# Performance work log

Measured on AMD Instinct MI355X. Metric: run time of the kernel, lower is better.

The kernel has to match this reference:

```python
import jax, jax.numpy as jnp
import numpy as np

B, S, NH, HID, NL = 64, 512, 16, 512, 16
W_WIN, PAD, THR, BW = 5, 2, 5.0, 0.1
D_IN = 1 + 2 * NH


def setup_inputs():
    key = jax.random.key(0)
    ks = jax.random.split(key, 16)
    time = jax.random.uniform(ks[0], (B, S)) * 1000.0
    mag = 15.0 + jax.random.normal(ks[1], (B, S))
    err = 0.01 + 0.1 * jax.random.uniform(ks[2], (B, S))
    sc = 0.05
    p = {}
    p["light_curve"] = jnp.stack([time, mag, err], axis=1)  # (B,3,S)
    p["valid_mask"] = jnp.ones((B, S), dtype=bool)
    p["frequency"] = 0.5 + 4.5 * jax.random.uniform(ks[3], (B,))
    p["W_ih0"] = sc * jax.random.normal(ks[4], (3 * HID, D_IN))
    p["b_ih0"] = jnp.zeros((3 * HID,))
    p["W_hh0"] = sc * jax.random.normal(ks[5], (3 * HID, HID))
    p["b_hh0"] = jnp.zeros((3 * HID,))
    p["W_ih1"] = sc * jax.random.normal(ks[6], (3 * HID, HID))
    p["b_ih1"] = jnp.zeros((3 * HID,))
    p["W_hh1"] = sc * jax.random.normal(ks[7], (3 * HID, HID))
    p["b_hh1"] = jnp.zeros((3 * HID,))
    p["Wl1"] = sc * jax.random.normal(ks[8], (HID, HID))
    p["bl1"] = jnp.zeros((HID,))
    p["Wl2"] = sc * jax.random.normal(ks[9], (NL, HID))
    p["bl2"] = jnp.zeros((NL,))
    return p


def _flag_outliers(phase, mag):
    # Sorted-window weighted (Epanechnikov in circular phase-delta) mean/std outlier test.
    # Caller guarantees all points valid (setup uses an all-True mask), so index_select == identity.
    perm = jnp.argsort(phase)
    ps, ms = phase[perm], mag[perm]

    def windows(x):
        xp = jnp.concatenate([x[-PAD:], x, x[:PAD]])  # circular pad
        return jnp.stack([xp[i:i + S] for i in range(W_WIN)], axis=-1)  # (S, w)

    wp, wm = windows(ps), windows(ms)
    cols = jnp.array([i for i in range(W_WIN) if i != PAD])
    dphi = wp[:, cols] - wp[:, PAD:PAD + 1]
    dphi = jnp.remainder(dphi - 0.5, 1.0) - 0.5
    wgt = 0.75 * (1.0 - dphi ** 2)
    wmm = wm[:, cols]
    wsum = wgt.sum(-1)
    loc = (wmm * wgt).sum(-1) / wsum
    scale = jnp.sqrt((((wmm - loc[:, None]) ** 2) * wgt).sum(-1) / (wsum - 1.0))
    thr = loc + THR * scale
    sigma = jnp.zeros_like(mag).at[perm].set(thr)  # inverse-permute (index_copy_)
    return mag > sigma


def _gru_layer(x, W_ih, b_ih, W_hh, b_hh):
    # torch nn.GRU cell math; x: (B,S,D) -> (B,S,H)
    xW = jnp.einsum('bsd,gd->bsg', x, W_ih) + b_ih  # (B,S,3H)

    def step(h, xt):
        hW = h @ W_hh.T + b_hh
        xr, xz, xn = jnp.split(xt, 3, axis=-1)
        hr, hz, hn = jnp.split(hW, 3, axis=-1)
        r = jax.nn.sigmoid(xr + hr)
        z = jax.nn.sigmoid(xz + hz)
        n = jnp.tanh(xn + r * hn)
        h = (1.0 - z) * n + z * h
        return h, h

    h0 = jnp.zeros((x.shape[0], W_hh.shape[1]), x.dtype)
    _, hs = jax.lax.scan(step, h0, jnp.swapaxes(xW, 0, 1))
    return jnp.swapaxes(hs, 0, 1)


def reference(light_curve, valid_mask, frequency, W_ih0, b_ih0, W_hh0, b_hh0,
              W_ih1, b_ih1, W_hh1, b_hh1, Wl1, bl1, Wl2, bl2):
    time, mag, err = light_curve[:, 0], light_curve[:, 1], light_curve[:, 2]
    period = 2.0 / frequency[:, None]  # fold_with_double_period=True (default)
    phase = jnp.remainder(time, period) / period
    outlier = jax.vmap(_flag_outliers)(phase, mag)
    is_valid = valid_mask & ~outlier

    # periodic-kernel interpolation on 50-point grid; align phase to brightness max
    grid = jnp.linspace(0.0, 1.0, 50)
    delta = grid[None, :, None] - phase[:, None, :]  # (B,50,S)
    K = jnp.exp((jnp.cos(2.0 * jnp.pi * delta) - 1.0) / BW ** 2)
    Wk = is_valid[:, None, :].astype(K.dtype) * K
    Wk = Wk / Wk.sum(-1, keepdims=True)
    smooth = (Wk * mag[:, None, :]).sum(-1)  # (B,50)
    phase = phase - grid[jnp.argmax(smooth, axis=-1)][:, None]

    # sort by phase, invalid points last; scaler=None -> loc 0, scale 1
    big = jnp.finfo(jnp.float32).max
    idx = jnp.argsort(jnp.where(is_valid, phase, big), axis=-1)
    phase = jnp.take_along_axis(phase, idx, -1)
    mag = jnp.take_along_axis(mag, idx, -1)
    is_valid = jnp.take_along_axis(is_valid, idx, -1)

    # Fourier phase embedding [cos_1..cos_H, sin_1..sin_H] + mag -> (B,S,2H+1)
    k = jnp.arange(1, NH + 1, dtype=phase.dtype)
    ang = 2.0 * jnp.pi * phase[:, :, None] * k
    emb = jnp.concatenate([jnp.cos(ang), jnp.sin(ang), mag[:, :, None]], axis=-1)

    ht = _gru_layer(emb, W_ih0, b_ih0, W_hh0, b_hh0)
    ht = _gru_layer(ht, W_ih1, b_ih1, W_hh1, b_hh1)

    m = is_valid[:, :, None].astype(ht.dtype)  # context='average'
    ctx = (ht * m).sum(1) / m.sum(1)
    h1 = jax.nn.gelu(ctx @ Wl1.T + bl1, approximate=False)
    z = h1 @ Wl2.T + bl2
    return z
```

## Files before the change

### kernel.cpp

```cpp
#include <hip/hip_runtime.h>


typedef unsigned short u16;
typedef unsigned int u32;
typedef unsigned long long u64;

__device__ __forceinline__ float b2f(u16 u) { return __uint_as_float(((u32)u) << 16); }
__device__ __forceinline__ float blo(u32 u) { return __uint_as_float(u << 16); }
__device__ __forceinline__ float bhi(u32 u) { return __uint_as_float(u & 0xffff0000u); }
__device__ __forceinline__ u16 f2b(float f) {
    u32 x = __float_as_uint(f);
    u32 r = x + 0x7fffu + ((x >> 16) & 1u);
    return (u16)(r >> 16);
}

#define SS 512
#define TWO_PI 6.28318530717958647692f
#define BIGF 3.402823466e+38f
#define PANEL_ELEMS (1536 * 512)
#define FLAGS_BYTES 32768
#define RD 4

struct P {
    const void* lc;
    const void* freq;
    const void* W[12];
    void* out;
    void* ws;
    unsigned long long ws_size;
};

__device__ __forceinline__ bool inputs_are_bf16(const void* freq) {
    const u16* q = (const u16*)freq;
    bool ok = true;
    for (int i = 0; i < 64; ++i) {
        float v = b2f(q[i]);
        ok = ok && (v >= 0.4f) && (v <= 5.5f);
    }
    return ok;
}

template<bool BF>
__device__ __forceinline__ float ldw(const void* p, size_t i) {
    if constexpr (BF) return b2f(((const u16*)p)[i]);
    else              return ((const float*)p)[i];
}
template<bool BF>
__device__ __forceinline__ const void* rowp(const void* base, int row) {
    if constexpr (BF) return (const void*)((const u16*)base + (size_t)row * 512);
    else              return (const void*)((const float*)base + (size_t)row * 512);
}

__device__ __forceinline__ void sc_store_f(float* ptr, float v) {
    __hip_atomic_store(ptr, v, __ATOMIC_RELAXED, __HIP_MEMORY_SCOPE_AGENT);
}
__device__ __forceinline__ float sc_load_f(const float* ptr) {
    return __hip_atomic_load(ptr, __ATOMIC_RELAXED, __HIP_MEMORY_SCOPE_AGENT);
}
__device__ __forceinline__ void sc_store_i(int* ptr, int v) {
    __hip_atomic_store(ptr, v, __ATOMIC_RELAXED, __HIP_MEMORY_SCOPE_AGENT);
}
__device__ __forceinline__ int sc_load_i(const int* ptr) {
    return __hip_atomic_load(ptr, __ATOMIC_RELAXED, __HIP_MEMORY_SCOPE_AGENT);
}

__device__ __forceinline__ void waitge(const int* f, int v, int* dead) {
    if (*dead) return;
    int it = 0;
    while (sc_load_i(f) < v) {
        __builtin_amdgcn_s_sleep(1);
        if (++it > 2000000) { *dead = 1; break; }
    }
}

template<bool BF>
__device__ void build_panel_one(const void* W, int tid, char* panbase) {
    if constexpr (BF) {
        const uint4* Ws = (const uint4*)W;
        uint4* panel = (uint4*)panbase;
        for (int i = tid; i < 1536 * 64; i += 512) {
            int r = i >> 6, k8 = i & 63;
            panel[(size_t)k8 * 1536 + r] = Ws[i];
        }
    } else {
        const float4* Ws = (const float4*)W;
        float4* panel = (float4*)panbase;
        for (int i = tid; i < 1536 * 128; i += 512) {
            int r = i >> 7, k4 = i & 127;
            panel[(size_t)k4 * 1536 + r] = Ws[i];
        }
    }
}

template<bool BF>
__device__ __forceinline__ void tridot_panel(const void* panel, int j,
                                             const float* __restrict__ sh,
                                             float& ar, float& az, float& an) {
    if constexpr (BF) {
        const uint4* pr = (const uint4*)panel + j;
        const uint4* pz = pr + 512;
        const uint4* pn = pr + 1024;
        for (int k0 = 0; k0 < 512; k0 += 8) {
            size_t o = (size_t)(k0 >> 3) * 1536;
            float4 h0 = *(const float4*)&sh[k0];
            float4 h1 = *(const float4*)&sh[k0 + 4];
            uint4 a = pr[o], c = pz[o], d = pn[o];
            ar += blo(a.x) * h0.x + bhi(a.x) * h0.y + blo(a.y) * h0.z + bhi(a.y) * h0.w
                + blo(a.z) * h1.x + bhi(a.z) * h1.y + blo(a.w) * h1.z + bhi(a.w) * h1.w;
            az += blo(c.x) * h0.x + bhi(c.x) * h0.y + blo(c.y) * h0.z + bhi(c.y) * h0.w
                + blo(c.z) * h1.x + bhi(c.z) * h1.y + blo(c.w) * h1.z + bhi(c.w) * h1.w;
            an += blo(d.x) * h0.x + bhi(d.x) * h0.y + blo(d.y) * h0.z + bhi(d.y) * h0.w
                + blo(d.z) * h1.x + bhi(d.z) * h1.y + blo(d.w) * h1.z + bhi(d.w) * h1.w;
        }
    } else {
        const float4* pr = (const float4*)panel + j;
        const float4* pz = pr + 512;
        const float4* pn = pr + 1024;
        for (int k0 = 0; k0 < 512; k0 += 8) {
            size_t o = (size_t)(k0 >> 2) * 1536;
            float4 h0 = *(const float4*)&sh[k0];
            float4 h1 = *(const float4*)&sh[k0 + 4];
            float4 a0 = pr[o], a1 = pr[o + 1536];
            float4 c0 = pz[o], c1 = pz[o + 1536];
            float4 d0 = pn[o], d1 = pn[o + 1536];
            ar += a0.x * h0.x + a0.y * h0.y + a0.z * h0.z + a0.w * h0.w
                + a1.x * h1.x + a1.y * h1.y + a1.z * h1.z + a1.w * h1.w;
            az += c0.x * h0.x + c0.y * h0.y + c0.z * h0.z + c0.w * h0.w
                + c1.x * h1.x + c1.y * h1.y + c1.z * h1.z + c1.w * h1.w;
            an += d0.x * h0.x + d0.y * h0.y + d0.z * h0.z + d0.w * h0.w
                + d1.x * h1.x + d1.y * h1.y + d1.z * h1.z + d1.w * h1.w;
        }
    }
}

template<bool BF>
__device__ __forceinline__ float dot512(const void* vr, const float* __restrict__ sh) {
    float acc = 0.f;
    if constexpr (BF) {
        const u32* pr = (const u32*)vr;
        for (int k0 = 0; k0 < 512; k0 += 8) {
            float4 h0 = *(const float4*)&sh[k0];
            float4 h1 = *(const float4*)&sh[k0 + 4];
            uint4 a = *(const uint4*)(pr + (k0 >> 1));
            acc += blo(a.x) * h0.x + bhi(a.x) * h0.y + blo(a.y) * h0.z + bhi(a.y) * h0.w
                 + blo(a.z) * h1.x + bhi(a.z) * h1.y + blo(a.w) * h1.z + bhi(a.w) * h1.w;
        }
    } else {
        const float* pr = (const float*)vr;
        for (int k0 = 0; k0 < 512; k0 += 8) {
            float4 h0 = *(const float4*)&sh[k0];
            float4 h1 = *(const float4*)&sh[k0 + 4];
            float4 a0 = *(const float4*)(pr + k0), a1 = *(const float4*)(pr + k0 + 4);
            acc += a0.x * h0.x + a0.y * h0.y + a0.z * h0.z + a0.w * h0.w
                 + a1.x * h1.x + a1.y * h1.y + a1.z * h1.z + a1.w * h1.w;
        }
    }
    return acc;
}

struct PreShm {
    float ph[512], mg[512], skey[512], sig[512], vld[512];
    int   sidx[512];
    float ps2[512], ms2[512], vs2[512];
    float pn[50][8], pd[50][8], smoothv[50];
    float gshift, nv;
};

__device__ void bitonic512(float* skey, int* sidx, int tid) {
    for (int k = 2; k <= 512; k <<= 1) {
        for (int j = k >> 1; j > 0; j >>= 1) {
            int ixj = tid ^ j;
            if (ixj > tid) {
                float ka = skey[tid], kb = skey[ixj];
                int ia = sidx[tid], ib = sidx[ixj];
                bool up = ((tid & k) == 0);
                bool agtb = (ka > kb) || (ka == kb && ia > ib);
                if (agtb == up) {
                    skey[tid] = kb; skey[ixj] = ka;
                    sidx[tid] = ib; sidx[ixj] = ia;
                }
            }
            __syncthreads();
        }
    }
}

template<bool BF>
__device__ void preproc_core(const P& p, PreShm& s, int b, int tid) {
    float period = 2.0f / ldw<BF>(p.freq, b);
    float t = ldw<BF>(p.lc, (size_t)b * 3 * SS + tid);
    float m = ldw<BF>(p.lc, (size_t)b * 3 * SS + SS + tid);
    float ph0 = fmodf(t, period) / period;
    s.ph[tid] = ph0; s.mg[tid] = m;
    s.skey[tid] = ph0; s.sidx[tid] = tid;
    __syncthreads();
    bitonic512(s.skey, s.sidx, tid);
    {
        float pc = s.skey[tid];
        float wv[4], mv[4];
        float wsum = 0.f, wm = 0.f;
        const int offs[4] = {-2, -1, 1, 2};
#pragma unroll
        for (int c = 0; c < 4; ++c) {
            int jj = (tid + offs[c]) & 511;
            float d = s.skey[jj] - pc;
            float u = d - 0.5f; u = u - floorf(u);
            float dphi = u - 0.5f;
            float w = 0.75f * (1.0f - dphi * dphi);
            float mm = s.mg[s.sidx[jj]];
            wv[c] = w; mv[c] = mm;
            wsum += w; wm += w * mm;
        }
        float loc = wm / wsum;
        float s2 = 0.f;
#pragma unroll
        for (int c = 0; c < 4; ++c) { float dm = mv[c] - loc; s2 += dm * dm * wv[c]; }
        float scale = sqrtf(s2 / (wsum - 1.0f));
        s.sig[s.sidx[tid]] = loc + 5.0f * scale;
    }
    __syncthreads();
    s.vld[tid] = (s.mg[tid] > s.sig[tid]) ? 0.0f : 1.0f;
    __syncthreads();
    if (tid == 0) {
        float acc = 0.f;
        for (int i = 0; i < 512; ++i) acc += s.vld[i];
        s.nv = acc;
    }
    {
        int g = tid >> 3, pq = tid & 7;
        if (g < 50) {
            float gv = (float)g * (1.0f / 49.0f);
            float num = 0.f, den = 0.f;
            int s0 = pq * 64;
            for (int ss = s0; ss < s0 + 64; ++ss) {
                float d = gv - s.ph[ss];
                float c = cosf(TWO_PI * d);
                float K = expf((c - 1.0f) * 100.0f);
                float w = s.vld[ss] * K;
                den += w; num += w * s.mg[ss];
            }
            s.pn[g][pq] = num; s.pd[g][pq] = den;
        }
    }
    __syncthreads();
    if (tid < 50) {
        float num = 0.f, den = 0.f;
#pragma unroll
        for (int c = 0; c < 8; ++c) { num += s.pn[tid][c]; den += s.pd[tid][c]; }
        s.smoothv[tid] = num / den;
    }
    __syncthreads();
    if (tid == 0) {
        float best = s.smoothv[0]; int bi = 0;
        for (int g = 1; g < 50; ++g) if (s.smoothv[g] > best) { best = s.smoothv[g]; bi = g; }
        s.gshift = (float)bi * (1.0f / 49.0f);
    }
    __syncthreads();
    float p2 = s.ph[tid] - s.gshift;
    s.ph[tid] = p2;
    s.skey[tid] = (s.vld[tid] > 0.f) ? p2 : BIGF;
    s.sidx[tid] = tid;
    __syncthreads();
    bitonic512(s.skey, s.sidx, tid);
    {
        int o = s.sidx[tid];
        s.ps2[tid] = s.ph[o]; s.ms2[tid] = s.mg[o]; s.vs2[tid] = s.vld[o];
    }
    __syncthreads();
}

struct ShmU {
    union {
        struct { PreShm pre; float h0[512], h1[512], eL[34]; } a;
        struct { float h0loc[512]; } b;
        struct { float vs2[512], h1[512], cg[1024], nv; } c;
    } u;
    int dead;
};

template<bool BF, bool PAN>
__device__ void run_all(const P& p, ShmU& S) {
    PreShm& pre = S.u.a.pre;
    float* h0 = S.u.a.h0;
    float* h1 = S.u.a.h1;
    float* eL = S.u.a.eL;
    int b = blockIdx.x, tid = threadIdx.x;
    char* panbase = (char*)p.ws + FLAGS_BYTES;
    const size_t PMAT = (size_t)PANEL_ELEMS * (BF ? 2 : 4);

    if constexpr (PAN) {
        build_panel_one<BF>(p.W[2], tid, panbase);
        build_panel_one<BF>(p.W[4], tid, panbase + PMAT);
        build_panel_one<BF>(p.W[6], tid, panbase + 2 * PMAT);
        __threadfence();
    }
    preproc_core<BF>(p, pre, b, tid);

    int j = tid;
    float wr0[33], wz0[33], wn0[33];
#pragma unroll
    for (int d = 0; d < 33; ++d) {
        wr0[d] = ldw<BF>(p.W[0], (size_t)j * 33 + d);
        wz0[d] = ldw<BF>(p.W[0], ((size_t)j + 512) * 33 + d);
        wn0[d] = ldw<BF>(p.W[0], ((size_t)j + 1024) * 33 + d);
    }
    float bi0r = ldw<BF>(p.W[1], j), bi0z = ldw<BF>(p.W[1], j + 512), bi0n = ldw<BF>(p.W[1], j + 1024);
    float bh0r = ldw<BF>(p.W[3], j), bh0z = ldw<BF>(p.W[3], j + 512), bh0n = ldw<BF>(p.W[3], j + 1024);
    float bi1r = ldw<BF>(p.W[5], j), bi1z = ldw<BF>(p.W[5], j + 512), bi1n = ldw<BF>(p.W[5], j + 1024);
    float bh1r = ldw<BF>(p.W[7], j), bh1z = ldw<BF>(p.W[7], j + 512), bh1n = ldw<BF>(p.W[7], j + 1024);

    const void* pan0  = (const void*)panbase;
    const void* pan1x = (const void*)(panbase + PMAT);
    const void* pan1h = (const void*)(panbase + 2 * PMAT);
    const void *w0r = rowp<BF>(p.W[2], j), *w0z = rowp<BF>(p.W[2], j + 512), *w0n = rowp<BF>(p.W[2], j + 1024);
    const void *x1r = rowp<BF>(p.W[4], j), *x1z = rowp<BF>(p.W[4], j + 512), *x1n = rowp<BF>(p.W[4], j + 1024);
    const void *w1r = rowp<BF>(p.W[6], j), *w1z = rowp<BF>(p.W[6], j + 512), *w1n = rowp<BF>(p.W[6], j + 1024);

    h0[j] = 0.f; h1[j] = 0.f;
    float cacc = 0.f;
    __syncthreads();

    for (int tt = 0; tt < 512; ++tt) {
        if (j < 16) {
            float ang = TWO_PI * pre.ps2[tt] * (float)(j + 1);
            float sv, cv; sincosf(ang, &sv, &cv);
            eL[j] = cv; eL[16 + j] = sv;
        }
        if (j == 32) eL[32] = pre.ms2[tt];
        __syncthreads();
        float xr = bi0r, xz = bi0z, xn = bi0n;
#pragma unroll
        for (int d = 0; d < 33; ++d) {
            float e = eL[d];
            xr += wr0[d] * e; xz += wz0[d] * e; xn += wn0[d] * e;
        }
        float ar = bh0r, az = bh0z, an = bh0n;
        if constexpr (PAN) tridot_panel<BF>(pan0, j, h0, ar, az, an);
        else {
            for (int k = 0; k < 512; ++k) {
                float h = h0[k];
                ar += ldw<BF>(w0r, k) * h; az += ldw<BF>(w0z, k) * h; an += ldw<BF>(w0n, k) * h;
            }
        }
        float h0prev = h0[j];
        float r0 = 1.0f / (1.0f + expf(-(xr + ar)));
        float z0 = 1.0f / (1.0f + expf(-(xz + az)));
        float n0 = tanhf(xn + r0 * an);
        float nh0 = (1.0f - z0) * n0 + z0 * h0prev;
        __syncthreads();
        h0[j] = nh0;
        __syncthreads();
        float yr = bi1r, yz = bi1z, yn = bi1n;
        float cr = bh1r, cz = bh1z, cn = bh1n;
        if constexpr (PAN) {
            tridot_panel<BF>(pan1x, j, h0, yr, yz, yn);
            tridot_panel<BF>(pan1h, j, h1, cr, cz, cn);
        } else {
            for (int k = 0; k < 512; ++k) {
                float h = h0[k], g = h1[k];
                yr += ldw<BF>(x1r, k) * h; yz += ldw<BF>(x1z, k) * h; yn += ldw<BF>(x1n, k) * h;
                cr += ldw<BF>(w1r, k) * g; cz += ldw<BF>(w1z, k) * g; cn += ldw<BF>(w1n, k) * g;
            }
        }
        float h1prev = h1[j];
        float r1 = 1.0f / (1.0f + expf(-(yr + cr)));
        float z1 = 1.0f / (1.0f + expf(-(yz + cz)));
        float n1 = tanhf(yn + r1 * cn);
        float nh1 = (1.0f - z1) * n1 + z1 * h1prev;
        cacc += pre.vs2[tt] * nh1;
        __syncthreads();
        h1[j] = nh1;
    }
    __syncthreads();

    h0[j] = cacc / pre.nv;
    __syncthreads();
    float a1 = ldw<BF>(p.W[9], j) + dot512<BF>(rowp<BF>(p.W[8], j), h0);
    float g = 0.5f * a1 * (1.0f + erff(a1 * 0.70710678118654752440f));
    __syncthreads();
    h1[j] = g;
    __syncthreads();
    if (j < 16) {
        float a2 = ldw<BF>(p.W[11], j) + dot512<BF>(rowp<BF>(p.W[10], j), h1);
        if constexpr (BF) ((u16*)p.out)[(size_t)b * 16 + j] = f2b(a2);
        else              ((float*)p.out)[(size_t)b * 16 + j] = a2;
    }
}

__global__ __launch_bounds__(512) void fused_kernel_old(P p) {
    __shared__ ShmU S;
    bool bf = inputs_are_bf16(p.freq);
    u64 PMAT = bf ? 1572864ull : 3145728ull;
    bool pan = (p.ws && p.ws_size >= (u64)FLAGS_BYTES + 3 * PMAT);
    if (bf) { if (pan) run_all<true, true>(p, S);  else run_all<true, false>(p, S); }
    else    { if (pan) run_all<false, true>(p, S); else run_all<false, false>(p, S); }
}


template<bool BF>
__device__ void runA(const P& p, ShmU& S, int b, int tid,
                     char* panbase, float* h0r, float* vs2g, float* nvg, int* flags) {
    build_panel_one<BF>(p.W[2], tid, panbase);
    __threadfence();
    preproc_core<BF>(p, S.u.a.pre, b, tid);
    sc_store_f(&vs2g[(size_t)b * 512 + tid], S.u.a.pre.vs2[tid]);
    if (tid == 0) sc_store_f(&nvg[b], S.u.a.pre.nv);
    asm volatile("s_waitcnt vmcnt(0)" ::: "memory");
    __syncthreads();
    if (tid == 0) { S.dead = 0; sc_store_i(&flags[4096 + b * 16], 1); }

    int j = tid;
    float wr0[33], wz0[33], wn0[33];
#pragma unroll
    for (int d = 0; d < 33; ++d) {
        wr0[d] = ldw<BF>(p.W[0], (size_t)j * 33 + d);
        wz0[d] = ldw<BF>(p.W[0], ((size_t)j + 512) * 33 + d);
        wn0[d] = ldw<BF>(p.W[0], ((size_t)j + 1024) * 33 + d);
    }
    float bi0r = ldw<BF>(p.W[1], j), bi0z = ldw<BF>(p.W[1], j + 512), bi0n = ldw<BF>(p.W[1], j + 1024);
    float bh0r = ldw<BF>(p.W[3], j), bh0z = ldw<BF>(p.W[3], j + 512), bh0n = ldw<BF>(p.W[3], j + 1024);

    float* h0 = S.u.a.h0;
    float* eL = S.u.a.eL;
    h0[j] = 0.f;
    __syncthreads();

    for (int t = 0; t < 512; ++t) {
        if (j < 16) {
            float ang = TWO_PI * S.u.a.pre.ps2[t] * (float)(j + 1);
            float sv, cv; sincosf(ang, &sv, &cv);
            eL[j] = cv; eL[16 + j] = sv;
        }
        if (j == 32) eL[32] = S.u.a.pre.ms2[t];
        __syncthreads();
        float xr = bi0r, xz = bi0z, xn = bi0n;
#pragma unroll
        for (int d = 0; d < 33; ++d) {
            float e = eL[d];
            xr += wr0[d] * e; xz += wz0[d] * e; xn += wn0[d] * e;
        }
        float ar = bh0r, az = bh0z, an = bh0n;
        tridot_panel<BF>(panbase, j, h0, ar, az, an);
        float h0prev = h0[j];
        float r0 = 1.0f / (1.0f + expf(-(xr + ar)));
        float z0 = 1.0f / (1.0f + expf(-(xz + az)));
        float n0 = tanhf(xn + r0 * an);
        float nh0 = (1.0f - z0) * n0 + z0 * h0prev;
        __syncthreads();
        h0[j] = nh0;
        if (tid == 0 && t >= RD) waitge(&flags[1024 + b * 16], t - RD + 1, &S.dead);
        __syncthreads();
        sc_store_f(&h0r[((size_t)b * RD + (t & (RD - 1))) * 512 + j], nh0);
        asm volatile("s_waitcnt vmcnt(0)" ::: "memory");
        __syncthreads();
        if (tid == 0) sc_store_i(&flags[b * 16], t + 1);
    }
}

template<bool BF>
__device__ void runB(const P& p, ShmU& S, int b, int tid,
                     char* panbase, float* h0r, float* yrng, int* flags) {
    build_panel_one<BF>(p.W[4], tid, panbase);
    __threadfence();
    if (tid == 0) S.dead = 0;
    __syncthreads();

    int j = tid;
    float bi1r = ldw<BF>(p.W[5], j), bi1z = ldw<BF>(p.W[5], j + 512), bi1n = ldw<BF>(p.W[5], j + 1024);
    float* h0loc = S.u.b.h0loc;

    for (int t = 0; t < 512; ++t) {
        if (tid == 0) {
            waitge(&flags[b * 16], t + 1, &S.dead);
            if (t >= RD) waitge(&flags[3072 + b * 16], t - RD + 1, &S.dead);
        }
        __syncthreads();
        h0loc[tid] = sc_load_f(&h0r[((size_t)b * RD + (t & (RD - 1))) * 512 + tid]);
        __syncthreads();
        if (tid == 0) sc_store_i(&flags[1024 + b * 16], t + 1);
        float yr = bi1r, yz = bi1z, yn = bi1n;
        tridot_panel<BF>(panbase, j, h0loc, yr, yz, yn);
        float* slot = &yrng[((size_t)b * RD + (t & (RD - 1))) * 1536];
        sc_store_f(&slot[j], yr);
        sc_store_f(&slot[512 + j], yz);
        sc_store_f(&slot[1024 + j], yn);
        asm volatile("s_waitcnt vmcnt(0)" ::: "memory");
        __syncthreads();
        if (tid == 0) sc_store_i(&flags[2048 + b * 16], t + 1);
    }
}

template<bool BF>
__device__ void runC(const P& p, ShmU& S, int b, int tid,
                     char* panbase, float* yrng, float* vs2g, float* nvg, int* flags) {
    build_panel_one<BF>(p.W[6], tid, panbase);
    __threadfence();
    if (tid == 0) S.dead = 0;
    __syncthreads();
    if (tid == 0) waitge(&flags[4096 + b * 16], 1, &S.dead);
    __syncthreads();
    S.u.c.vs2[tid] = sc_load_f(&vs2g[(size_t)b * 512 + tid]);
    if (tid == 0) S.u.c.nv = sc_load_f(&nvg[b]);
    S.u.c.h1[tid] = 0.f;
    __syncthreads();

    int j = tid;
    float bh1r = ldw<BF>(p.W[7], j), bh1z = ldw<BF>(p.W[7], j + 512), bh1n = ldw<BF>(p.W[7], j + 1024);
    float* h1 = S.u.c.h1;
    float cacc = 0.f;

    for (int t = 0; t < 512; ++t) {
        if (tid == 0) waitge(&flags[2048 + b * 16], t + 1, &S.dead);
        __syncthreads();
        const float* slot = &yrng[((size_t)b * RD + (t & (RD - 1))) * 1536];
        float yr = sc_load_f(&slot[j]);
        float yz = sc_load_f(&slot[512 + j]);
        float yn = sc_load_f(&slot[1024 + j]);
        float cr = bh1r, cz = bh1z, cn = bh1n;
        tridot_panel<BF>(panbase, j, h1, cr, cz, cn);
        float h1prev = h1[j];
        float r1 = 1.0f / (1.0f + expf(-(yr + cr)));
        float z1 = 1.0f / (1.0f + expf(-(yz + cz)));
        float n1 = tanhf(yn + r1 * cn);
        float nh1 = (1.0f - z1) * n1 + z1 * h1prev;
        cacc += S.u.c.vs2[t] * nh1;
        __syncthreads();
        h1[j] = nh1;
        if (tid == 0) sc_store_i(&flags[3072 + b * 16], t + 1);
        __syncthreads();
    }

    float* ctxL = &S.u.c.cg[0];
    float* gL   = &S.u.c.cg[512];
    ctxL[j] = cacc / S.u.c.nv;
    __syncthreads();
    float a1 = ldw<BF>(p.W[9], j) + dot512<BF>(rowp<BF>(p.W[8], j), ctxL);
    float g = 0.5f * a1 * (1.0f + erff(a1 * 0.70710678118654752440f));
    __syncthreads();
    gL[j] = g;
    __syncthreads();
    if (j < 16) {
        float a2 = ldw<BF>(p.W[11], j) + dot512<BF>(rowp<BF>(p.W[10], j), gL);
        if constexpr (BF) ((u16*)p.out)[(size_t)b * 16 + j] = f2b(a2);
        else              ((float*)p.out)[(size_t)b * 16 + j] = a2;
    }
}

template<bool BF>
__device__ void run_pipe(const P& p, ShmU& S) {
    const int bid = blockIdx.x;
    const int role = bid % 3, b = bid / 3;
    const int tid = threadIdx.x;

    char* wsb = (char*)p.ws;
    int* flags = (int*)wsb;
    const size_t PMAT = (size_t)PANEL_ELEMS * (BF ? 2 : 4);
    char* pan0  = wsb + FLAGS_BYTES;
    char* pan1x = pan0 + PMAT;
    char* pan1h = pan0 + 2 * PMAT;
    float* h0r  = (float*)(pan0 + 3 * PMAT);
    float* yrng = h0r + (size_t)64 * RD * 512;
    float* vs2g = yrng + (size_t)64 * RD * 1536;
    float* nvg  = vs2g + (size_t)64 * 512;

    if (role == 0)      runA<BF>(p, S, b, tid, pan0, h0r, vs2g, nvg, flags);
    else if (role == 1) runB<BF>(p, S, b, tid, pan1x, h0r, yrng, flags);
    else                runC<BF>(p, S, b, tid, pan1h, yrng, vs2g, nvg, flags);
}

__global__ __launch_bounds__(512) void fused_kernel_pipe(P p) {
    __shared__ ShmU S;
    if (inputs_are_bf16(p.freq)) run_pipe<true>(p, S);
    else                         run_pipe<false>(p, S);
}

extern "C" void kernel_launch(void* const* d_in, const int* in_sizes, int n_in,
                              void* d_out, int out_size, void* d_ws, size_t ws_size,
                              hipStream_t stream) {
    P p;
    p.lc = d_in[0];
    p.freq = d_in[2];
    for (int i = 0; i < 12; ++i) p.W[i] = d_in[3 + i];
    p.out = d_out;
    p.ws = d_ws;
    p.ws_size = (unsigned long long)ws_size;

    const size_t need_pipe = 32768ull + 9437184ull + 524288ull + 1572864ull + 131072ull + 4096ull;
    if (d_ws && ws_size >= need_pipe) {
        hipMemsetAsync(d_ws, 0, FLAGS_BYTES, stream);
        fused_kernel_pipe<<<192, 512, 0, stream>>>(p);
    } else {
        fused_kernel_old<<<64, 512, 0, stream>>>(p);
    }
    (void)in_sizes; (void)n_in; (void)out_size;
}
```

Before: 14.87 ms.

## Split each GRU stage across two blocks processing two batch rows per group

```diff
diff --git a/kernel.cpp b/kernel.cpp
--- a/kernel.cpp
+++ b/kernel.cpp
@@ -19,7 +19,15 @@
 #define BIGF 3.402823466e+38f
 #define PANEL_ELEMS (1536 * 512)
 #define FLAGS_BYTES 32768
-#define RD 4
+#define FL(g, f) (((g) * 16 + (f)) * 16)
+#define F_A 0
+#define F_B 2
+#define F_C 4
+#define G_A 6
+#define G_B 8
+#define G_C 10
+#define F_PRE 12
+#define F_CTX 14
 
 struct P {
     const void* lc;
@@ -63,7 +71,6 @@
 __device__ __forceinline__ int sc_load_i(const int* ptr) {
     return __hip_atomic_load(ptr, __ATOMIC_RELAXED, __HIP_MEMORY_SCOPE_AGENT);
 }
-
 __device__ __forceinline__ void waitge(const int* f, int v, int* dead) {
     if (*dead) return;
     int it = 0;
@@ -88,6 +95,28 @@
         for (int i = tid; i < 1536 * 128; i += 512) {
             int r = i >> 7, k4 = i & 127;
             panel[(size_t)k4 * 1536 + r] = Ws[i];
+        }
+    }
+}
+template<bool BF>
+__device__ void build_piece(const void* W, int half, int tid, char* panbase) {
+    if constexpr (BF) {
+        const uint4* Ws = (const uint4*)W;
+        uint4* panel = (uint4*)panbase;
+        for (int i = tid; i < 768 * 64; i += 512) {
+            int r768 = i >> 6, k8 = i & 63;
+            int g3 = r768 >> 8, r = r768 & 255;
+            int srcrow = g3 * 512 + half * 256 + r;
+            panel[(size_t)k8 * 768 + r768] = Ws[(size_t)srcrow * 64 + k8];
+        }
+    } else {
+        const float4* Ws = (const float4*)W;
+        float4* panel = (float4*)panbase;
+        for (int i = tid; i < 768 * 128; i += 512) {
+            int r768 = i >> 7, k4 = i & 127;
+            int g3 = r768 >> 8, r = r768 & 255;
+            int srcrow = g3 * 512 + half * 256 + r;
+            panel[(size_t)k4 * 768 + r768] = Ws[(size_t)srcrow * 128 + k4];
         }
     }
 }
@@ -134,6 +163,47 @@
 }
 
 template<bool BF>
+__device__ __forceinline__ void tridot_piece(const void* panel, int r,
+                                             const float* __restrict__ sh,
+                                             float& ar, float& az, float& an) {
+    if constexpr (BF) {
+        const uint4* pr = (const uint4*)panel + r;
+        const uint4* pz = pr + 256;
+        const uint4* pn = pr + 512;
+        for (int k0 = 0; k0 < 512; k0 += 8) {
+            size_t o = (size_t)(k0 >> 3) * 768;
+            float4 h0 = *(const float4*)&sh[k0];
+            float4 h1 = *(const float4*)&sh[k0 + 4];
+            uint4 a = pr[o], c = pz[o], d = pn[o];
+            ar += blo(a.x) * h0.x + bhi(a.x) * h0.y + blo(a.y) * h0.z + bhi(a.y) * h0.w
+                + blo(a.z) * h1.x + bhi(a.z) * h1.y + blo(a.w) * h1.z + bhi(a.w) * h1.w;
+            az += blo(c.x) * h0.x + bhi(c.x) * h0.y + blo(c.y) * h0.z + bhi(c.y) * h0.w
+                + blo(c.z) * h1.x + bhi(c.z) * h1.y + blo(c.w) * h1.z + bhi(c.w) * h1.w;
+            an += blo(d.x) * h0.x + bhi(d.x) * h0.y + blo(d.y) * h0.z + bhi(d.y) * h0.w
+                + blo(d.z) * h1.x + bhi(d.z) * h1.y + blo(d.w) * h1.z + bhi(d.w) * h1.w;
+        }
+    } else {
+        const float4* pr = (const float4*)panel + r;
+        const float4* pz = pr + 256;
+        const float4* pn = pr + 512;
+        for (int k0 = 0; k0 < 512; k0 += 8) {
+            size_t o = (size_t)(k0 >> 2) * 768;
+            float4 h0 = *(const float4*)&sh[k0];
+            float4 h1 = *(const float4*)&sh[k0 + 4];
+            float4 a0 = pr[o], a1 = pr[o + 768];
+            float4 c0 = pz[o], c1 = pz[o + 768];
+            float4 d0 = pn[o], d1 = pn[o + 768];
+            ar += a0.x * h0.x + a0.y * h0.y + a0.z * h0.z + a0.w * h0.w
+                + a1.x * h1.x + a1.y * h1.y + a1.z * h1.z + a1.w * h1.w;
+            az += c0.x * h0.x + c0.y * h0.y + c0.z * h0.z + c0.w * h0.w
+                + c1.x * h1.x + c1.y * h1.y + c1.z * h1.z + c1.w * h1.w;
+            an += d0.x * h0.x + d0.y * h0.y + d0.z * h0.z + d0.w * h0.w
+                + d1.x * h1.x + d1.y * h1.y + d1.z * h1.z + d1.w * h1.w;
+        }
+    }
+}
+
+template<bool BF>
 __device__ __forceinline__ float dot512(const void* vr, const float* __restrict__ sh) {
     float acc = 0.f;
     if constexpr (BF) {
@@ -269,21 +339,21 @@
     __syncthreads();
 }
 
+struct ShmA { PreShm pre; float psb[2][512], msb[2][512]; float h0L[1024]; float eL[2][34]; };
+struct ShmB { float h0loc[1024]; };
+struct ShmC { float h1L[1024]; float vs2L[2][512]; float nvL[2]; float ctxL[512], gL[512]; };
+struct ShmOldA { PreShm pre; float h0[512], h1[512], eL[34]; };
 struct ShmU {
-    union {
-        struct { PreShm pre; float h0[512], h1[512], eL[34]; } a;
-        struct { float h0loc[512]; } b;
-        struct { float vs2[512], h1[512], cg[1024], nv; } c;
-    } u;
+    union { ShmA a; ShmB b; ShmC c; ShmOldA o; } u;
     int dead;
 };
 
 template<bool BF, bool PAN>
 __device__ void run_all(const P& p, ShmU& S) {
-    PreShm& pre = S.u.a.pre;
-    float* h0 = S.u.a.h0;
-    float* h1 = S.u.a.h1;
-    float* eL = S.u.a.eL;
+    PreShm& pre = S.u.o.pre;
+    float* h0 = S.u.o.h0;
+    float* h1 = S.u.o.h1;
+    float* eL = S.u.o.eL;
     int b = blockIdx.x, tid = threadIdx.x;
     char* panbase = (char*)p.ws + FLAGS_BYTES;
     const size_t PMAT = (size_t)PANEL_ELEMS * (BF ? 2 : 4);
@@ -398,18 +468,28 @@
 
 
 template<bool BF>
-__device__ void runA(const P& p, ShmU& S, int b, int tid,
-                     char* panbase, float* h0r, float* vs2g, float* nvg, int* flags) {
-    build_panel_one<BF>(p.W[2], tid, panbase);
+__device__ void runA(const P& p, ShmU& S, int g, int hf, int tid, char* pan,
+                     float* h0r, float* pp, int* flags) {
+    build_piece<BF>(p.W[2], hf, tid, pan);
     __threadfence();
-    preproc_core<BF>(p, S.u.a.pre, b, tid);
-    sc_store_f(&vs2g[(size_t)b * 512 + tid], S.u.a.pre.vs2[tid]);
-    if (tid == 0) sc_store_f(&nvg[b], S.u.a.pre.nv);
+    int myb = 2 * g + hf, ob = 2 * g + (1 - hf);
+    preproc_core<BF>(p, S.u.a.pre, myb, tid);
+    sc_store_f(&pp[(size_t)myb * 2048 + tid], S.u.a.pre.ps2[tid]);
+    sc_store_f(&pp[(size_t)myb * 2048 + 512 + tid], S.u.a.pre.ms2[tid]);
+    sc_store_f(&pp[(size_t)myb * 2048 + 1024 + tid], S.u.a.pre.vs2[tid]);
+    if (tid == 0) sc_store_f(&pp[(size_t)myb * 2048 + 1536], S.u.a.pre.nv);
     asm volatile("s_waitcnt vmcnt(0)" ::: "memory");
     __syncthreads();
-    if (tid == 0) { S.dead = 0; sc_store_i(&flags[4096 + b * 16], 1); }
-
-    int j = tid;
+    if (tid == 0) sc_store_i(&flags[FL(g, F_PRE + hf)], 1);
+    S.u.a.psb[hf][tid] = S.u.a.pre.ps2[tid];
+    S.u.a.msb[hf][tid] = S.u.a.pre.ms2[tid];
+    if (tid == 0) waitge(&flags[FL(g, F_PRE + (1 - hf))], 1, &S.dead);
+    __syncthreads();
+    S.u.a.psb[1 - hf][tid] = sc_load_f(&pp[(size_t)ob * 2048 + tid]);
+    S.u.a.msb[1 - hf][tid] = sc_load_f(&pp[(size_t)ob * 2048 + 512 + tid]);
+
+    const int r = tid & 255, bb = tid >> 8;
+    const int j = hf * 256 + r;
     float wr0[33], wz0[33], wn0[33];
 #pragma unroll
     for (int d = 0; d < 33; ++d) {
@@ -420,152 +500,202 @@
     float bi0r = ldw<BF>(p.W[1], j), bi0z = ldw<BF>(p.W[1], j + 512), bi0n = ldw<BF>(p.W[1], j + 1024);
     float bh0r = ldw<BF>(p.W[3], j), bh0z = ldw<BF>(p.W[3], j + 512), bh0n = ldw<BF>(p.W[3], j + 1024);
 
-    float* h0 = S.u.a.h0;
-    float* eL = S.u.a.eL;
-    h0[j] = 0.f;
+    S.u.a.h0L[tid] = 0.f; S.u.a.h0L[tid + 512] = 0.f;
     __syncthreads();
 
     for (int t = 0; t < 512; ++t) {
-        if (j < 16) {
-            float ang = TWO_PI * S.u.a.pre.ps2[t] * (float)(j + 1);
+        if (t > 0) {
+            if (tid == 0) waitge(&flags[FL(g, F_A + (1 - hf))], t, &S.dead);
+            __syncthreads();
+            S.u.a.h0L[bb * 512 + (1 - hf) * 256 + r] =
+                sc_load_f(&h0r[(size_t)g * 2048 + ((t - 1) & 1) * 1024 + (1 - hf) * 512 + bb * 256 + r]);
+            __syncthreads();
+            if (tid == 0) sc_store_i(&flags[FL(g, G_A + hf)], t);
+        }
+        if (tid < 16) {
+            float ang = TWO_PI * S.u.a.psb[0][t] * (float)(tid + 1);
             float sv, cv; sincosf(ang, &sv, &cv);
-            eL[j] = cv; eL[16 + j] = sv;
-        }
-        if (j == 32) eL[32] = S.u.a.pre.ms2[t];
+            S.u.a.eL[0][tid] = cv; S.u.a.eL[0][16 + tid] = sv;
+        } else if (tid < 32) {
+            int k = tid - 16;
+            float ang = TWO_PI * S.u.a.psb[1][t] * (float)(k + 1);
+            float sv, cv; sincosf(ang, &sv, &cv);
+            S.u.a.eL[1][k] = cv; S.u.a.eL[1][16 + k] = sv;
+        }
+        if (tid == 32) S.u.a.eL[0][32] = S.u.a.msb[0][t];
+        if (tid == 33) S.u.a.eL[1][32] = S.u.a.msb[1][t];
         __syncthreads();
         float xr = bi0r, xz = bi0z, xn = bi0n;
 #pragma unroll
         for (int d = 0; d < 33; ++d) {
-            float e = eL[d];
+            float e = S.u.a.eL[bb][d];
             xr += wr0[d] * e; xz += wz0[d] * e; xn += wn0[d] * e;
         }
         float ar = bh0r, az = bh0z, an = bh0n;
-        tridot_panel<BF>(panbase, j, h0, ar, az, an);
-        float h0prev = h0[j];
+        tridot_piece<BF>(pan, r, &S.u.a.h0L[bb * 512], ar, az, an);
+        float h0prev = S.u.a.h0L[bb * 512 + j];
         float r0 = 1.0f / (1.0f + expf(-(xr + ar)));
         float z0 = 1.0f / (1.0f + expf(-(xz + az)));
         float n0 = tanhf(xn + r0 * an);
         float nh0 = (1.0f - z0) * n0 + z0 * h0prev;
         __syncthreads();
-        h0[j] = nh0;
-        if (tid == 0 && t >= RD) waitge(&flags[1024 + b * 16], t - RD + 1, &S.dead);
-        __syncthreads();
-        sc_store_f(&h0r[((size_t)b * RD + (t & (RD - 1))) * 512 + j], nh0);
+        S.u.a.h0L[bb * 512 + j] = nh0;
+        if (tid == 0 && t >= 2) {
+            waitge(&flags[FL(g, G_A + (1 - hf))], t - 1, &S.dead);
+            waitge(&flags[FL(g, G_B + 0)], t - 1, &S.dead);
+            waitge(&flags[FL(g, G_B + 1)], t - 1, &S.dead);
+        }
+        __syncthreads();
+        sc_store_f(&h0r[(size_t)g * 2048 + (t & 1) * 1024 + hf * 512 + bb * 256 + r], nh0);
         asm volatile("s_waitcnt vmcnt(0)" ::: "memory");
         __syncthreads();
-        if (tid == 0) sc_store_i(&flags[b * 16], t + 1);
-    }
-}
-
-template<bool BF>
-__device__ void runB(const P& p, ShmU& S, int b, int tid,
-                     char* panbase, float* h0r, float* yrng, int* flags) {
-    build_panel_one<BF>(p.W[4], tid, panbase);
+        if (tid == 0) sc_store_i(&flags[FL(g, F_A + hf)], t + 1);
+    }
+}
+
+template<bool BF>
+__device__ void runB(const P& p, ShmU& S, int g, int hf, int tid, char* pan,
+                     float* h0r, float* yrng, int* flags) {
+    build_piece<BF>(p.W[4], hf, tid, pan);
     __threadfence();
-    if (tid == 0) S.dead = 0;
-    __syncthreads();
-
-    int j = tid;
+    __syncthreads();
+    const int r = tid & 255, bb = tid >> 8;
+    const int j = hf * 256 + r;
     float bi1r = ldw<BF>(p.W[5], j), bi1z = ldw<BF>(p.W[5], j + 512), bi1n = ldw<BF>(p.W[5], j + 1024);
-    float* h0loc = S.u.b.h0loc;
 
     for (int t = 0; t < 512; ++t) {
         if (tid == 0) {
-            waitge(&flags[b * 16], t + 1, &S.dead);
-            if (t >= RD) waitge(&flags[3072 + b * 16], t - RD + 1, &S.dead);
-        }
-        __syncthreads();
-        h0loc[tid] = sc_load_f(&h0r[((size_t)b * RD + (t & (RD - 1))) * 512 + tid]);
-        __syncthreads();
-        if (tid == 0) sc_store_i(&flags[1024 + b * 16], t + 1);
+            waitge(&flags[FL(g, F_A + 0)], t + 1, &S.dead);
+            waitge(&flags[FL(g, F_A + 1)], t + 1, &S.dead);
+        }
+        __syncthreads();
+        S.u.b.h0loc[bb * 512 + r] =
+            sc_load_f(&h0r[(size_t)g * 2048 + (t & 1) * 1024 + 0 * 512 + bb * 256 + r]);
+        S.u.b.h0loc[bb * 512 + 256 + r] =
+            sc_load_f(&h0r[(size_t)g * 2048 + (t & 1) * 1024 + 1 * 512 + bb * 256 + r]);
+        __syncthreads();
+        if (tid == 0) sc_store_i(&flags[FL(g, G_B + hf)], t + 1);
         float yr = bi1r, yz = bi1z, yn = bi1n;
-        tridot_panel<BF>(panbase, j, h0loc, yr, yz, yn);
-        float* slot = &yrng[((size_t)b * RD + (t & (RD - 1))) * 1536];
-        sc_store_f(&slot[j], yr);
-        sc_store_f(&slot[512 + j], yz);
-        sc_store_f(&slot[1024 + j], yn);
+        tridot_piece<BF>(pan, r, &S.u.b.h0loc[bb * 512], yr, yz, yn);
+        if (tid == 0 && t >= 2) waitge(&flags[FL(g, G_C + hf)], t - 1, &S.dead);
+        __syncthreads();
+        float* slot = &yrng[(size_t)g * 6144 + (t & 1) * 3072 + hf * 1536];
+        sc_store_f(&slot[bb * 256 + r], yr);
+        sc_store_f(&slot[512 + bb * 256 + r], yz);
+        sc_store_f(&slot[1024 + bb * 256 + r], yn);
         asm volatile("s_waitcnt vmcnt(0)" ::: "memory");
         __syncthreads();
-        if (tid == 0) sc_store_i(&flags[2048 + b * 16], t + 1);
-    }
-}
-
-template<bool BF>
-__device__ void runC(const P& p, ShmU& S, int b, int tid,
-                     char* panbase, float* yrng, float* vs2g, float* nvg, int* flags) {
-    build_panel_one<BF>(p.W[6], tid, panbase);
+        if (tid == 0) sc_store_i(&flags[FL(g, F_B + hf)], t + 1);
+    }
+}
+
+template<bool BF>
+__device__ void runC(const P& p, ShmU& S, int g, int hf, int tid, char* pan,
+                     float* yrng, float* h1r, float* pp, float* ctxb, int* flags) {
+    build_piece<BF>(p.W[6], hf, tid, pan);
     __threadfence();
-    if (tid == 0) S.dead = 0;
-    __syncthreads();
-    if (tid == 0) waitge(&flags[4096 + b * 16], 1, &S.dead);
-    __syncthreads();
-    S.u.c.vs2[tid] = sc_load_f(&vs2g[(size_t)b * 512 + tid]);
-    if (tid == 0) S.u.c.nv = sc_load_f(&nvg[b]);
-    S.u.c.h1[tid] = 0.f;
-    __syncthreads();
-
-    int j = tid;
+    if (tid == 0) {
+        waitge(&flags[FL(g, F_PRE + 0)], 1, &S.dead);
+        waitge(&flags[FL(g, F_PRE + 1)], 1, &S.dead);
+    }
+    __syncthreads();
+    S.u.c.vs2L[0][tid] = sc_load_f(&pp[(size_t)(2 * g) * 2048 + 1024 + tid]);
+    S.u.c.vs2L[1][tid] = sc_load_f(&pp[(size_t)(2 * g + 1) * 2048 + 1024 + tid]);
+    if (tid == 0) {
+        S.u.c.nvL[0] = sc_load_f(&pp[(size_t)(2 * g) * 2048 + 1536]);
+        S.u.c.nvL[1] = sc_load_f(&pp[(size_t)(2 * g + 1) * 2048 + 1536]);
+    }
+    S.u.c.h1L[tid] = 0.f; S.u.c.h1L[tid + 512] = 0.f;
+    __syncthreads();
+
+    const int r = tid & 255, bb = tid >> 8;
+    const int j = hf * 256 + r;
     float bh1r = ldw<BF>(p.W[7], j), bh1z = ldw<BF>(p.W[7], j + 512), bh1n = ldw<BF>(p.W[7], j + 1024);
-    float* h1 = S.u.c.h1;
     float cacc = 0.f;
 
     for (int t = 0; t < 512; ++t) {
-        if (tid == 0) waitge(&flags[2048 + b * 16], t + 1, &S.dead);
-        __syncthreads();
-        const float* slot = &yrng[((size_t)b * RD + (t & (RD - 1))) * 1536];
-        float yr = sc_load_f(&slot[j]);
-        float yz = sc_load_f(&slot[512 + j]);
-        float yn = sc_load_f(&slot[1024 + j]);
+        if (tid == 0) {
+            waitge(&flags[FL(g, F_B + hf)], t + 1, &S.dead);
+            if (t > 0) waitge(&flags[FL(g, F_C + (1 - hf))], t, &S.dead);
+        }
+        __syncthreads();
+        if (t > 0) {
+            S.u.c.h1L[bb * 512 + (1 - hf) * 256 + r] =
+                sc_load_f(&h1r[(size_t)g * 2048 + ((t - 1) & 1) * 1024 + (1 - hf) * 512 + bb * 256 + r]);
+        }
+        const float* slot = &yrng[(size_t)g * 6144 + (t & 1) * 3072 + hf * 1536];
+        float yr = sc_load_f(&slot[bb * 256 + r]);
+        float yz = sc_load_f(&slot[512 + bb * 256 + r]);
+        float yn = sc_load_f(&slot[1024 + bb * 256 + r]);
+        __syncthreads();
+        if (tid == 0) sc_store_i(&flags[FL(g, G_C + hf)], t + 1);
         float cr = bh1r, cz = bh1z, cn = bh1n;
-        tridot_panel<BF>(panbase, j, h1, cr, cz, cn);
-        float h1prev = h1[j];
+        tridot_piece<BF>(pan, r, &S.u.c.h1L[bb * 512], cr, cz, cn);
+        float h1prev = S.u.c.h1L[bb * 512 + j];
         float r1 = 1.0f / (1.0f + expf(-(yr + cr)));
         float z1 = 1.0f / (1.0f + expf(-(yz + cz)));
         float n1 = tanhf(yn + r1 * cn);
         float nh1 = (1.0f - z1) * n1 + z1 * h1prev;
-        cacc += S.u.c.vs2[t] * nh1;
-        __syncthreads();
-        h1[j] = nh1;
-        if (tid == 0) sc_store_i(&flags[3072 + b * 16], t + 1);
-        __syncthreads();
-    }
-
-    float* ctxL = &S.u.c.cg[0];
-    float* gL   = &S.u.c.cg[512];
-    ctxL[j] = cacc / S.u.c.nv;
-    __syncthreads();
-    float a1 = ldw<BF>(p.W[9], j) + dot512<BF>(rowp<BF>(p.W[8], j), ctxL);
-    float g = 0.5f * a1 * (1.0f + erff(a1 * 0.70710678118654752440f));
-    __syncthreads();
-    gL[j] = g;
-    __syncthreads();
-    if (j < 16) {
-        float a2 = ldw<BF>(p.W[11], j) + dot512<BF>(rowp<BF>(p.W[10], j), gL);
-        if constexpr (BF) ((u16*)p.out)[(size_t)b * 16 + j] = f2b(a2);
-        else              ((float*)p.out)[(size_t)b * 16 + j] = a2;
+        cacc += S.u.c.vs2L[bb][t] * nh1;
+        __syncthreads();
+        S.u.c.h1L[bb * 512 + j] = nh1;
+        if (tid == 0 && t >= 2) waitge(&flags[FL(g, G_C + (1 - hf))], t - 1, &S.dead);
+        __syncthreads();
+        sc_store_f(&h1r[(size_t)g * 2048 + (t & 1) * 1024 + hf * 512 + bb * 256 + r], nh1);
+        asm volatile("s_waitcnt vmcnt(0)" ::: "memory");
+        __syncthreads();
+        if (tid == 0) sc_store_i(&flags[FL(g, F_C + hf)], t + 1);
+    }
+
+    sc_store_f(&ctxb[(size_t)g * 1024 + hf * 512 + bb * 256 + r], cacc);
+    asm volatile("s_waitcnt vmcnt(0)" ::: "memory");
+    __syncthreads();
+    if (tid == 0) {
+        sc_store_i(&flags[FL(g, F_CTX + hf)], 1);
+        waitge(&flags[FL(g, F_CTX + (1 - hf))], 1, &S.dead);
+    }
+    __syncthreads();
+    float nv = S.u.c.nvL[hf];
+    S.u.c.ctxL[tid] = sc_load_f(&ctxb[(size_t)g * 1024 + (tid >> 8) * 512 + hf * 256 + (tid & 255)]) / nv;
+    __syncthreads();
+    float a1 = ldw<BF>(p.W[9], tid) + dot512<BF>(rowp<BF>(p.W[8], tid), S.u.c.ctxL);
+    float gg = 0.5f * a1 * (1.0f + erff(a1 * 0.70710678118654752440f));
+    __syncthreads();
+    S.u.c.gL[tid] = gg;
+    __syncthreads();
+    if (tid < 16) {
+        float a2 = ldw<BF>(p.W[11], tid) + dot512<BF>(rowp<BF>(p.W[10], tid), S.u.c.gL);
+        int hb = 2 * g + hf;
+        if constexpr (BF) ((u16*)p.out)[(size_t)hb * 16 + tid] = f2b(a2);
+        else              ((float*)p.out)[(size_t)hb * 16 + tid] = a2;
     }
 }
 
 template<bool BF>
 __device__ void run_pipe(const P& p, ShmU& S) {
     const int bid = blockIdx.x;
-    const int role = bid % 3, b = bid / 3;
+    const int piece = bid & 7;
+    if (piece >= 6) return;
+    const int g = bid >> 3;
+    const int role = piece >> 1, hf = piece & 1;
     const int tid = threadIdx.x;
+    if (tid == 0) S.dead = 0;
+    __syncthreads();
 
     char* wsb = (char*)p.ws;
     int* flags = (int*)wsb;
-    const size_t PMAT = (size_t)PANEL_ELEMS * (BF ? 2 : 4);
-    char* pan0  = wsb + FLAGS_BYTES;
-    char* pan1x = pan0 + PMAT;
-    char* pan1h = pan0 + 2 * PMAT;
-    float* h0r  = (float*)(pan0 + 3 * PMAT);
-    float* yrng = h0r + (size_t)64 * RD * 512;
-    float* vs2g = yrng + (size_t)64 * RD * 1536;
-    float* nvg  = vs2g + (size_t)64 * 512;
-
-    if (role == 0)      runA<BF>(p, S, b, tid, pan0, h0r, vs2g, nvg, flags);
-    else if (role == 1) runB<BF>(p, S, b, tid, pan1x, h0r, yrng, flags);
-    else                runC<BF>(p, S, b, tid, pan1h, yrng, vs2g, nvg, flags);
+    const size_t PIECE = BF ? 786432 : 1572864;
+    char* pans = wsb + FLAGS_BYTES;
+    char* mypan = pans + (size_t)piece * PIECE;
+    float* h0r  = (float*)(pans + 6 * PIECE);
+    float* yrng = h0r + (size_t)32 * 2048;
+    float* h1r  = yrng + (size_t)32 * 6144;
+    float* pp   = h1r + (size_t)32 * 2048;
+    float* ctxb = pp + (size_t)64 * 2048;
+
+    if (role == 0)      runA<BF>(p, S, g, hf, tid, mypan, h0r, pp, flags);
+    else if (role == 1) runB<BF>(p, S, g, hf, tid, mypan, h0r, yrng, flags);
+    else                runC<BF>(p, S, g, hf, tid, mypan, yrng, h1r, pp, ctxb, flags);
 }
 
 __global__ __launch_bounds__(512) void fused_kernel_pipe(P p) {
@@ -585,10 +715,10 @@
     p.ws = d_ws;
     p.ws_size = (unsigned long long)ws_size;
 
-    const size_t need_pipe = 32768ull + 9437184ull + 524288ull + 1572864ull + 131072ull + 4096ull;
+    const size_t need_pipe = 11436032ull;
     if (d_ws && ws_size >= need_pipe) {
         hipMemsetAsync(d_ws, 0, FLAGS_BYTES, stream);
-        fused_kernel_pipe<<<192, 512, 0, stream>>>(p);
+        fused_kernel_pipe<<<256, 512, 0, stream>>>(p);
     } else {
         fused_kernel_old<<<64, 512, 0, stream>>>(p);
     }
```

After: 14.31 ms. -3.7%, faster.
